# Kernel tuning notes

Measured on AMD Instinct MI355X. Metric: run time of the kernel, lower is better.

The kernel has to match this reference:

```python
import jax, jax.numpy as jnp
import numpy as np

INPUT_DIM = 2048
N_TREES = 15
TREE_DEPTH = 3
N_LEAVES = 2 ** TREE_DEPTH          # 8
N_INTERNAL = 2 ** TREE_DEPTH - 1    # 7
PARAM_PER_TREE = N_INTERNAL * (INPUT_DIM + 1) + N_LEAVES * 2  # 14375
BATCH = 32768


def setup_inputs() -> dict:
    key = jax.random.key(0)
    k1, k2, k3 = jax.random.split(key, 3)
    x = jax.random.normal(k1, (BATCH, INPUT_DIM), dtype=jnp.float32)
    tree_params = jax.random.normal(k2, (1, N_TREES * PARAM_PER_TREE), dtype=jnp.float32)
    tree_weights = jax.random.uniform(k3, (1, N_TREES), dtype=jnp.float32)
    return {"x": x, "tree_params": tree_params, "tree_weights": tree_weights}


def reference(x, tree_params, tree_weights):
    D, T, I, L = INPUT_DIM, N_TREES, N_INTERNAL, N_LEAVES
    B = x.shape[0]
    p = tree_params[0].reshape(T, PARAM_PER_TREE)
    split_w = p[:, : I * D].reshape(T, I, D)                       # [T, I, D]
    split_b = p[:, I * D : I * (D + 1)]                            # [T, I]
    leaf_logits = p[:, I * (D + 1) :].reshape(T, L, 2)             # [T, L, 2]

    # One fused GEMM over all trees/nodes: [B, T, I]
    decisions = jax.nn.sigmoid(jnp.einsum('bd,tid->bti', x, split_w) + split_b)

    # Faithful replication of the original gating loop (leaf 0 ungated,
    # internal nodes with child index >= L are no-ops).
    leaf_probs = jnp.ones((B, T, L), dtype=x.dtype)
    for i in range(I):
        left, right = 2 * i + 1, 2 * i + 2
        d = decisions[:, :, i]
        if left < L:
            leaf_probs = leaf_probs.at[:, :, left].multiply(d)
        if right < L:
            leaf_probs = leaf_probs.at[:, :, right].multiply(1.0 - d)

    leaf_probs = leaf_probs / (leaf_probs.sum(axis=-1, keepdims=True) + 1e-8)
    leaf_dist = jax.nn.softmax(leaf_logits, axis=-1)               # [T, L, 2]
    tree_out = jnp.einsum('btl,tlc->btc', leaf_probs, leaf_dist)   # [B, T, 2]
    final_probs = jnp.einsum('btc,t->bc', tree_out, tree_weights[0])
    return final_probs
```

## Files before the change

### kernel.cpp

```cpp
#include <hip/hip_runtime.h>
#include <stdint.h>

#define D_IN    2048
#define NT      15
#define PPT     14359
#define NVALID  60

typedef __bf16   bf16x8 __attribute__((ext_vector_type(8)));
typedef float    f32x4  __attribute__((ext_vector_type(4)));
typedef uint32_t u32x4  __attribute__((ext_vector_type(4)));

#define WAITV(n) asm volatile("s_waitcnt vmcnt(" #n ")" ::: "memory")
#define WAITL0   asm volatile("s_waitcnt lgkmcnt(0)" ::: "memory")
#define SCHEDB   __builtin_amdgcn_sched_barrier(0)

#define CVT_PAIR(P, Q, HW, LW) do {                                   \
    uint32_t _up = __float_as_uint(P), _uq = __float_as_uint(Q);      \
    uint32_t _mp = _up & 0xFFFF0000u, _mq = _uq & 0xFFFF0000u;        \
    (HW) = (_up >> 16) | _mq;                                         \
    float _lp = (P) - __uint_as_float(_mp);                           \
    float _lq = (Q) - __uint_as_float(_mq);                           \
    (LW) = (__float_as_uint(_lp) >> 16) |                             \
           (__float_as_uint(_lq) & 0xFFFF0000u);                      \
  } while (0)

__device__ __forceinline__ void cvt8(const f32x4 A, const f32x4 B,
                                     u32x4& hi, u32x4& lo) {
  CVT_PAIR(A[0], A[1], hi[0], lo[0]);
  CVT_PAIR(A[2], A[3], hi[1], lo[1]);
  CVT_PAIR(B[0], B[1], hi[2], lo[2]);
  CVT_PAIR(B[2], B[3], hi[3], lo[3]);
}

__global__ __launch_bounds__(256) void prep_split(const float* __restrict__ tp,
                                                  const float* __restrict__ tw,
                                                  unsigned short* __restrict__ bsp,
                                                  float* __restrict__ bias,
                                                  float* __restrict__ coef) {
  const int n  = blockIdx.x;
  const int j  = threadIdx.x;
  const int k0 = j * 8;
  f32x4 v0 = {0,0,0,0}, v1 = {0,0,0,0};
  if (n < NVALID) {
    const float* src = tp + (size_t)(n >> 2) * PPT + (n & 3) * D_IN + k0;
#pragma unroll
    for (int q = 0; q < 4; ++q) v0[q] = src[q];
#pragma unroll
    for (int q = 0; q < 4; ++q) v1[q] = src[4 + q];
  }
  u32x4 hi, lo;
  cvt8(v0, v1, hi, lo);
  const int ks = k0 >> 5, f = n >> 4;
  const int lane = (n & 15) | (((k0 >> 3) & 3) << 4);
  char* bb = (char*)bsp + ((size_t)(ks * 4 + f) * 2) * 1024 + (size_t)lane * 16;
  *(u32x4*)(bb)        = hi;
  *(u32x4*)(bb + 1024) = lo;

  if (blockIdx.x == 0) {
    int tid = threadIdx.x;
    if (tid < 64) {
      float b = 0.0f;
      if (tid < NVALID) { int t = tid >> 2, i = tid & 3; b = tp[t * PPT + 14336 + i]; }
      bias[tid] = b;
    } else if (tid < 64 + NT) {
      int t = tid - 64;
      const float* ll = tp + t * PPT + 14343;
      float d0[8], d1[8];
#pragma unroll
      for (int le = 0; le < 8; ++le) {
        float aa = ll[2 * le], bb2 = ll[2 * le + 1];
        float m = fmaxf(aa, bb2);
        float e0 = __expf(aa - m), e1 = __expf(bb2 - m);
        float inv = 1.0f / (e0 + e1);
        d0[le] = e0 * inv; d1[le] = e1 * inv;
      }
      float ww = tw[t];
      float* c = coef + t * 10;
      c[0] = ww * (d0[0] + d0[2] + d0[4] + d0[6]);
      c[1] = ww * (d1[0] + d1[2] + d1[4] + d1[6]);
      c[2] = ww * (d0[1] - d0[2]);
      c[3] = ww * (d1[1] - d1[2]);
      c[4] = ww * (d0[3] - d0[4]);
      c[5] = ww * (d1[3] - d1[4]);
      c[6] = ww * (d0[5] - d0[6]);
      c[7] = ww * (d1[5] - d1[6]);
      c[8] = ww * d0[7];
      c[9] = ww * d1[7];
    }
  }
}

__device__ __forceinline__ f32x4 gload4(const float* p) {
  f32x4 r;
  asm volatile("global_load_dwordx4 %0, %1, off" : "=v"(r) : "v"(p) : "memory");
  return r;
}
__device__ __forceinline__ u32x4 dsread16(uint32_t addr) {
  u32x4 r;
  asm volatile("ds_read_b128 %0, %1" : "=v"(r) : "v"(addr) : "memory");
  return r;
}
__device__ __forceinline__ void stage16(const void* g, void* l) {
  __builtin_amdgcn_global_load_lds(
      (const __attribute__((address_space(1))) void*)g,
      (__attribute__((address_space(3))) void*)l, 16, 0, 0);
}

#define ITERATION(tt, BUF, RC, WN, ISSUE)                                      \
  {                                                                            \
    WAITV(WN); SCHEDB;                                                         \
    __builtin_amdgcn_s_barrier();                                              \
    const uint32_t bb = sbase + (BUF) * 16384 + l16;                           \
    u32x4 bfr[16];                                                             \
    _Pragma("unroll")                                                          \
    for (int q = 0; q < 16; ++q) bfr[q] = dsread16(bb + q * 1024);             \
    u32x4 ah0, al0, ah1, al1;                                                  \
    cvt8(RC[0], RC[1], ah0, al0);                                              \
    cvt8(RC[2], RC[3], ah1, al1);                                              \
    WAITL0; SCHEDB;                                                            \
    if (ISSUE) {                                                               \
      const int t3 = (tt) + 3;                                                 \
      const char* gsrc = bspb + (size_t)t3 * 16384 + w4096l16;                 \
      char* ldst = sBgen + (((BUF) + 3) & 3) * 16384 + w4096;                  \
      _Pragma("unroll")                                                        \
      for (int q = 0; q < 4; ++q) stage16(gsrc + q * 1024, ldst + q * 1024);   \
      const float* ap = xbase + t3 * 64;                                       \
      RC[0] = gload4(ap);      RC[1] = gload4(ap + 4);                         \
      RC[2] = gload4(ap + 32); RC[3] = gload4(ap + 36);                        \
    }                                                                          \
    _Pragma("unroll")                                                          \
    for (int f = 0; f < 4; ++f) {                                              \
      bf16x8 bh = __builtin_bit_cast(bf16x8, bfr[f * 2]);                      \
      bf16x8 bl = __builtin_bit_cast(bf16x8, bfr[f * 2 + 1]);                  \
      bf16x8 Ah = __builtin_bit_cast(bf16x8, ah0);                             \
      bf16x8 Al = __builtin_bit_cast(bf16x8, al0);                             \
      acc[f] = __builtin_amdgcn_mfma_f32_16x16x32_bf16(Ah, bh, acc[f], 0,0,0); \
      acc[f] = __builtin_amdgcn_mfma_f32_16x16x32_bf16(Al, bh, acc[f], 0,0,0); \
      acc[f] = __builtin_amdgcn_mfma_f32_16x16x32_bf16(Ah, bl, acc[f], 0,0,0); \
    }                                                                          \
    _Pragma("unroll")                                                          \
    for (int f = 0; f < 4; ++f) {                                              \
      bf16x8 bh = __builtin_bit_cast(bf16x8, bfr[8 + f * 2]);                  \
      bf16x8 bl = __builtin_bit_cast(bf16x8, bfr[8 + f * 2 + 1]);              \
      bf16x8 Ah = __builtin_bit_cast(bf16x8, ah1);                             \
      bf16x8 Al = __builtin_bit_cast(bf16x8, al1);                             \
      acc[f] = __builtin_amdgcn_mfma_f32_16x16x32_bf16(Ah, bh, acc[f], 0,0,0); \
      acc[f] = __builtin_amdgcn_mfma_f32_16x16x32_bf16(Al, bh, acc[f], 0,0,0); \
      acc[f] = __builtin_amdgcn_mfma_f32_16x16x32_bf16(Ah, bl, acc[f], 0,0,0); \
    }                                                                          \
  }

__global__ __launch_bounds__(256) void tree_fused(
    const float* __restrict__ x,
    const unsigned short* __restrict__ bsp,
    const float* __restrict__ bias,
    const float* __restrict__ coef,
    float* __restrict__ out)
{
  __shared__ __align__(1024) unsigned char sB[4 * 16384];

  const int tid = threadIdx.x;
  const int w   = tid >> 6;
  const int l   = tid & 63;
  const int rl  = l & 15;
  const int g   = l >> 4;
  const int l16 = l * 16;
  const int w4096 = w * 4096;
  const int w4096l16 = w4096 + l16;

  const int rowTile = blockIdx.x * 64 + w * 16;
  const float* xbase = x + (size_t)(rowTile + rl) * D_IN + g * 8;
  const char* bspb = (const char*)bsp;
  char* sBgen = (char*)&sB[0];
  const uint32_t sbase = (uint32_t)(uintptr_t)sBgen;

  f32x4 acc[4] = {};
  f32x4 r0[4], r1[4], r2[4];

  {
#pragma unroll
    for (int s = 0; s < 3; ++s) {
      const char* gs = bspb + (size_t)s * 16384 + w4096l16;
      char* ld = sBgen + s * 16384 + w4096;
#pragma unroll
      for (int q = 0; q < 4; ++q) stage16(gs + q * 1024, ld + q * 1024);
      const float* ap = xbase + s * 64;
      f32x4* rr = (s == 0) ? r0 : (s == 1) ? r1 : r2;
      rr[0] = gload4(ap);      rr[1] = gload4(ap + 4);
      rr[2] = gload4(ap + 32); rr[3] = gload4(ap + 36);
    }
  }

  for (int tb = 0; tb < 24; tb += 12) {
    ITERATION(tb + 0,  0, r0, 16, 1);
    ITERATION(tb + 1,  1, r1, 16, 1);
    ITERATION(tb + 2,  2, r2, 16, 1);
    ITERATION(tb + 3,  3, r0, 16, 1);
    ITERATION(tb + 4,  0, r1, 16, 1);
    ITERATION(tb + 5,  1, r2, 16, 1);
    ITERATION(tb + 6,  2, r0, 16, 1);
    ITERATION(tb + 7,  3, r1, 16, 1);
    ITERATION(tb + 8,  0, r2, 16, 1);
    ITERATION(tb + 9,  1, r0, 16, 1);
    ITERATION(tb + 10, 2, r1, 16, 1);
    ITERATION(tb + 11, 3, r2, 16, 1);
  }
  ITERATION(24, 0, r0, 16, 1);
  ITERATION(25, 1, r1, 16, 1);
  ITERATION(26, 2, r2, 16, 1);
  ITERATION(27, 3, r0, 16, 1);
  ITERATION(28, 0, r1, 16, 1);
  ITERATION(29, 1, r2, 16, 0);
  ITERATION(30, 2, r0,  8, 0);
  ITERATION(31, 3, r1,  0, 0);

  float (*strips)[16][65] = (float (*)[16][65])sBgen;
#pragma unroll
  for (int f = 0; f < 4; ++f)
#pragma unroll
    for (int r = 0; r < 4; ++r)
      strips[w][4 * g + r][16 * f + rl] = acc[f][r];
  WAITL0;

  float o0 = 0.0f, o1 = 0.0f;
#pragma unroll
  for (int jt = 0; jt < 4; ++jt) {
    int t = g + 4 * jt;
    if (t < NT) {
      const float* cf = coef + t * 10;
      float dd[4];
#pragma unroll
      for (int i = 0; i < 4; ++i) {
        float z = strips[w][rl][4 * t + i] + bias[4 * t + i];
        dd[i] = 1.0f / (1.0f + __expf(-z));
      }
      float s = 1.0f / (4.0f + dd[3] + 1e-8f);
      o0 += s * (cf[0] + dd[0] * cf[2] + dd[1] * cf[4] + dd[2] * cf[6] + dd[3] * cf[8]);
      o1 += s * (cf[1] + dd[0] * cf[3] + dd[1] * cf[5] + dd[2] * cf[7] + dd[3] * cf[9]);
    }
  }
  o0 += __shfl_xor(o0, 16); o0 += __shfl_xor(o0, 32);
  o1 += __shfl_xor(o1, 16); o1 += __shfl_xor(o1, 32);
  if (l < 16) {
    ((float2*)out)[rowTile + rl] = make_float2(o0, o1);
  }
}

extern "C" void kernel_launch(void* const* d_in, const int* in_sizes, int n_in,
                              void* d_out, int out_size, void* d_ws, size_t ws_size,
                              hipStream_t stream) {
  (void)in_sizes; (void)n_in; (void)out_size; (void)ws_size;
  const float* x  = (const float*)d_in[0];
  const float* tp = (const float*)d_in[1];
  const float* tw = (const float*)d_in[2];
  float* out = (float*)d_out;

  unsigned short* bsp = (unsigned short*)d_ws;
  float* bias = (float*)((char*)d_ws + 524288);
  float* coef = (float*)((char*)d_ws + 524288 + 256);

  prep_split<<<64, 256, 0, stream>>>(tp, tw, bsp, bias, coef);
  tree_fused<<<512, 256, 0, stream>>>(x, bsp, bias, coef, out);
}
```

Before: 57.33 us.

## Split N dimension across two wave groups with 512-thread blocks and 3-stage buffer

Doubles the block to 8 waves. Each 16-row M tile is now shared by two waves, and each of those waves computes half of the 64 output columns, so accumulators and B-fragment registers per wave are halved. The LDS pipeline drops from 4 stages to 3 (prefetch distance 2 instead of 3), which frees shared memory and registers so more waves can be resident. In exchange, every x row is loaded and converted twice (once per N-half), a full __syncthreads is needed before the epilogue, and per-half partial outputs are reduced through LDS.

```diff
diff --git a/kernel.cpp b/kernel.cpp
--- a/kernel.cpp
+++ b/kernel.cpp
@@ -110,128 +110,120 @@
   {                                                                            \
     WAITV(WN); SCHEDB;                                                         \
     __builtin_amdgcn_s_barrier();                                              \
-    const uint32_t bb = sbase + (BUF) * 16384 + l16;                           \
-    u32x4 bfr[16];                                                             \
-    _Pragma("unroll")                                                          \
-    for (int q = 0; q < 16; ++q) bfr[q] = dsread16(bb + q * 1024);             \
+    const uint32_t bb = sbase + (BUF) * 16384 + n4096 + l16;                   \
+    u32x4 bfr[8];                                                              \
+    _Pragma("unroll")                                                          \
+    for (int q = 0; q < 4; ++q) bfr[q]     = dsread16(bb + q * 1024);          \
+    _Pragma("unroll")                                                          \
+    for (int q = 0; q < 4; ++q) bfr[4 + q] = dsread16(bb + 8192 + q * 1024);   \
     u32x4 ah0, al0, ah1, al1;                                                  \
     cvt8(RC[0], RC[1], ah0, al0);                                              \
     cvt8(RC[2], RC[3], ah1, al1);                                              \
     WAITL0; SCHEDB;                                                            \
     if (ISSUE) {                                                               \
-      const int t3 = (tt) + 3;                                                 \
-      const char* gsrc = bspb + (size_t)t3 * 16384 + w4096l16;                 \
-      char* ldst = sBgen + (((BUF) + 3) & 3) * 16384 + w4096;                  \
-      _Pragma("unroll")                                                        \
-      for (int q = 0; q < 4; ++q) stage16(gsrc + q * 1024, ldst + q * 1024);   \
-      const float* ap = xbase + t3 * 64;                                       \
+      const int t2 = (tt) + 2;                                                 \
+      const char* gsrc = bspb + (size_t)t2 * 16384 + w2048l16;                 \
+      char* ldst = sBgen + (((BUF) + 2) % 3) * 16384 + w2048;                  \
+      stage16(gsrc,        ldst);                                              \
+      stage16(gsrc + 1024, ldst + 1024);                                       \
+      const float* ap = xbase + t2 * 64;                                       \
       RC[0] = gload4(ap);      RC[1] = gload4(ap + 4);                         \
       RC[2] = gload4(ap + 32); RC[3] = gload4(ap + 36);                        \
     }                                                                          \
     _Pragma("unroll")                                                          \
-    for (int f = 0; f < 4; ++f) {                                              \
-      bf16x8 bh = __builtin_bit_cast(bf16x8, bfr[f * 2]);                      \
-      bf16x8 bl = __builtin_bit_cast(bf16x8, bfr[f * 2 + 1]);                  \
+    for (int ff = 0; ff < 2; ++ff) {                                           \
+      bf16x8 bh = __builtin_bit_cast(bf16x8, bfr[2 * ff]);                     \
+      bf16x8 bl = __builtin_bit_cast(bf16x8, bfr[2 * ff + 1]);                 \
       bf16x8 Ah = __builtin_bit_cast(bf16x8, ah0);                             \
       bf16x8 Al = __builtin_bit_cast(bf16x8, al0);                             \
-      acc[f] = __builtin_amdgcn_mfma_f32_16x16x32_bf16(Ah, bh, acc[f], 0,0,0); \
-      acc[f] = __builtin_amdgcn_mfma_f32_16x16x32_bf16(Al, bh, acc[f], 0,0,0); \
-      acc[f] = __builtin_amdgcn_mfma_f32_16x16x32_bf16(Ah, bl, acc[f], 0,0,0); \
+      acc[ff] = __builtin_amdgcn_mfma_f32_16x16x32_bf16(Ah, bh, acc[ff],0,0,0);\
+      acc[ff] = __builtin_amdgcn_mfma_f32_16x16x32_bf16(Al, bh, acc[ff],0,0,0);\
+      acc[ff] = __builtin_amdgcn_mfma_f32_16x16x32_bf16(Ah, bl, acc[ff],0,0,0);\
     }                                                                          \
     _Pragma("unroll")                                                          \
-    for (int f = 0; f < 4; ++f) {                                              \
-      bf16x8 bh = __builtin_bit_cast(bf16x8, bfr[8 + f * 2]);                  \
-      bf16x8 bl = __builtin_bit_cast(bf16x8, bfr[8 + f * 2 + 1]);              \
+    for (int ff = 0; ff < 2; ++ff) {                                           \
+      bf16x8 bh = __builtin_bit_cast(bf16x8, bfr[4 + 2 * ff]);                 \
+      bf16x8 bl = __builtin_bit_cast(bf16x8, bfr[4 + 2 * ff + 1]);             \
       bf16x8 Ah = __builtin_bit_cast(bf16x8, ah1);                             \
       bf16x8 Al = __builtin_bit_cast(bf16x8, al1);                             \
-      acc[f] = __builtin_amdgcn_mfma_f32_16x16x32_bf16(Ah, bh, acc[f], 0,0,0); \
-      acc[f] = __builtin_amdgcn_mfma_f32_16x16x32_bf16(Al, bh, acc[f], 0,0,0); \
-      acc[f] = __builtin_amdgcn_mfma_f32_16x16x32_bf16(Ah, bl, acc[f], 0,0,0); \
+      acc[ff] = __builtin_amdgcn_mfma_f32_16x16x32_bf16(Ah, bh, acc[ff],0,0,0);\
+      acc[ff] = __builtin_amdgcn_mfma_f32_16x16x32_bf16(Al, bh, acc[ff],0,0,0);\
+      acc[ff] = __builtin_amdgcn_mfma_f32_16x16x32_bf16(Ah, bl, acc[ff],0,0,0);\
     }                                                                          \
   }
 
-__global__ __launch_bounds__(256) void tree_fused(
+__global__ __launch_bounds__(512, 4) void tree_fused(
     const float* __restrict__ x,
     const unsigned short* __restrict__ bsp,
     const float* __restrict__ bias,
     const float* __restrict__ coef,
     float* __restrict__ out)
 {
-  __shared__ __align__(1024) unsigned char sB[4 * 16384];
+  __shared__ __align__(1024) unsigned char sB[3 * 16384];
 
   const int tid = threadIdx.x;
   const int w   = tid >> 6;
   const int l   = tid & 63;
   const int rl  = l & 15;
   const int g   = l >> 4;
+  const int m   = w & 3;
+  const int n   = w >> 2;
   const int l16 = l * 16;
-  const int w4096 = w * 4096;
-  const int w4096l16 = w4096 + l16;
-
-  const int rowTile = blockIdx.x * 64 + w * 16;
+  const int n4096 = n * 4096;
+  const int w2048 = w * 2048;
+  const int w2048l16 = w2048 + l16;
+
+  const int rowTile = blockIdx.x * 64 + m * 16;
   const float* xbase = x + (size_t)(rowTile + rl) * D_IN + g * 8;
   const char* bspb = (const char*)bsp;
   char* sBgen = (char*)&sB[0];
   const uint32_t sbase = (uint32_t)(uintptr_t)sBgen;
 
-  f32x4 acc[4] = {};
-  f32x4 r0[4], r1[4], r2[4];
+  f32x4 acc[2] = {};
+  f32x4 rA[4], rB[4];
 
   {
-#pragma unroll
-    for (int s = 0; s < 3; ++s) {
-      const char* gs = bspb + (size_t)s * 16384 + w4096l16;
-      char* ld = sBgen + s * 16384 + w4096;
-#pragma unroll
-      for (int q = 0; q < 4; ++q) stage16(gs + q * 1024, ld + q * 1024);
-      const float* ap = xbase + s * 64;
-      f32x4* rr = (s == 0) ? r0 : (s == 1) ? r1 : r2;
-      rr[0] = gload4(ap);      rr[1] = gload4(ap + 4);
-      rr[2] = gload4(ap + 32); rr[3] = gload4(ap + 36);
-    }
-  }
-
-  for (int tb = 0; tb < 24; tb += 12) {
-    ITERATION(tb + 0,  0, r0, 16, 1);
-    ITERATION(tb + 1,  1, r1, 16, 1);
-    ITERATION(tb + 2,  2, r2, 16, 1);
-    ITERATION(tb + 3,  3, r0, 16, 1);
-    ITERATION(tb + 4,  0, r1, 16, 1);
-    ITERATION(tb + 5,  1, r2, 16, 1);
-    ITERATION(tb + 6,  2, r0, 16, 1);
-    ITERATION(tb + 7,  3, r1, 16, 1);
-    ITERATION(tb + 8,  0, r2, 16, 1);
-    ITERATION(tb + 9,  1, r0, 16, 1);
-    ITERATION(tb + 10, 2, r1, 16, 1);
-    ITERATION(tb + 11, 3, r2, 16, 1);
-  }
-  ITERATION(24, 0, r0, 16, 1);
-  ITERATION(25, 1, r1, 16, 1);
-  ITERATION(26, 2, r2, 16, 1);
-  ITERATION(27, 3, r0, 16, 1);
-  ITERATION(28, 0, r1, 16, 1);
-  ITERATION(29, 1, r2, 16, 0);
-  ITERATION(30, 2, r0,  8, 0);
-  ITERATION(31, 3, r1,  0, 0);
-
-  float (*strips)[16][65] = (float (*)[16][65])sBgen;
-#pragma unroll
-  for (int f = 0; f < 4; ++f)
+    stage16(bspb + w2048l16,        sBgen + w2048);
+    stage16(bspb + w2048l16 + 1024, sBgen + w2048 + 1024);
+    rA[0] = gload4(xbase);      rA[1] = gload4(xbase + 4);
+    rA[2] = gload4(xbase + 32); rA[3] = gload4(xbase + 36);
+    stage16(bspb + 16384 + w2048l16,        sBgen + 16384 + w2048);
+    stage16(bspb + 16384 + w2048l16 + 1024, sBgen + 16384 + w2048 + 1024);
+    rB[0] = gload4(xbase + 64); rB[1] = gload4(xbase + 68);
+    rB[2] = gload4(xbase + 96); rB[3] = gload4(xbase + 100);
+  }
+
+  for (int tb = 0; tb < 30; tb += 6) {
+    ITERATION(tb + 0, 0, rA, 6, 1);
+    ITERATION(tb + 1, 1, rB, 6, 1);
+    ITERATION(tb + 2, 2, rA, 6, 1);
+    ITERATION(tb + 3, 0, rB, 6, 1);
+    ITERATION(tb + 4, 1, rA, 6, 1);
+    ITERATION(tb + 5, 2, rB, 6, 1);
+  }
+  ITERATION(30, 0, rA, 6, 0);
+  ITERATION(31, 1, rB, 0, 0);
+
+  float* sfl = (float*)sBgen;
+  float* pp  = (float*)(sBgen + 2 * 16384);
+
+#pragma unroll
+  for (int ff = 0; ff < 2; ++ff)
 #pragma unroll
     for (int r = 0; r < 4; ++r)
-      strips[w][4 * g + r][16 * f + rl] = acc[f][r];
-  WAITL0;
+      sfl[(m * 16 + 4 * g + r) * 64 + 32 * n + 16 * ff + rl] = acc[ff][r];
+  __syncthreads();
 
   float o0 = 0.0f, o1 = 0.0f;
 #pragma unroll
-  for (int jt = 0; jt < 4; ++jt) {
-    int t = g + 4 * jt;
+  for (int jt2 = 0; jt2 < 2; ++jt2) {
+    int t = g + 4 * (2 * n + jt2);
     if (t < NT) {
       const float* cf = coef + t * 10;
       float dd[4];
 #pragma unroll
       for (int i = 0; i < 4; ++i) {
-        float z = strips[w][rl][4 * t + i] + bias[4 * t + i];
+        float z = sfl[(m * 16 + rl) * 64 + 4 * t + i] + bias[4 * t + i];
         dd[i] = 1.0f / (1.0f + __expf(-z));
       }
       float s = 1.0f / (4.0f + dd[3] + 1e-8f);
@@ -242,7 +234,14 @@
   o0 += __shfl_xor(o0, 16); o0 += __shfl_xor(o0, 32);
   o1 += __shfl_xor(o1, 16); o1 += __shfl_xor(o1, 32);
   if (l < 16) {
-    ((float2*)out)[rowTile + rl] = make_float2(o0, o1);
+    pp[((m * 2 + n) * 16 + rl) * 2 + 0] = o0;
+    pp[((m * 2 + n) * 16 + rl) * 2 + 1] = o1;
+  }
+  __syncthreads();
+  if (n == 0 && l < 16) {
+    float a0 = pp[((m * 2) * 16 + rl) * 2 + 0] + pp[((m * 2 + 1) * 16 + rl) * 2 + 0];
+    float a1 = pp[((m * 2) * 16 + rl) * 2 + 1] + pp[((m * 2 + 1) * 16 + rl) * 2 + 1];
+    ((float2*)out)[rowTile + rl] = make_float2(a0, a1);
   }
 }
 
@@ -260,5 +259,5 @@
   float* coef = (float*)((char*)d_ws + 524288 + 256);
 
   prep_split<<<64, 256, 0, stream>>>(tp, tw, bsp, bias, coef);
-  tree_fused<<<512, 256, 0, stream>>>(x, bsp, bias, coef, out);
-}
+  tree_fused<<<512, 512, 0, stream>>>(x, bsp, bias, coef, out);
+}
```

After: 81.23 us. 41.7% more time.

## Swap operand staging: stream B into registers, stage x through swizzled LDS

Applied to the files above, without the earlier changes.

The weight tile (B) is now double-buffered directly in registers via global loads that every wave issues (each wave reads the full 16 KB per k-step), instead of being shared through LDS with block barriers. The x rows are staged per-wave into a 3-deep swizzled LDS ring via global_load_lds and read back with ds_read_b128. This removes the per-iteration s_barrier and the 16 LDS reads of B per step. In exchange it raises VGPR pressure (64 u32x4 registers for B buffers) and multiplies global and L2 traffic for B by four, which may hurt occupancy.

```diff
diff --git a/kernel.cpp b/kernel.cpp
--- a/kernel.cpp
+++ b/kernel.cpp
@@ -90,8 +90,13 @@
   }
 }
 
-__device__ __forceinline__ f32x4 gload4(const float* p) {
+__device__ __forceinline__ f32x4 gload4f(const float* p) {
   f32x4 r;
+  asm volatile("global_load_dwordx4 %0, %1, off" : "=v"(r) : "v"(p) : "memory");
+  return r;
+}
+__device__ __forceinline__ u32x4 gload4u(const char* p) {
+  u32x4 r;
   asm volatile("global_load_dwordx4 %0, %1, off" : "=v"(r) : "v"(p) : "memory");
   return r;
 }
@@ -106,47 +111,59 @@
       (__attribute__((address_space(3))) void*)l, 16, 0, 0);
 }
 
-#define ITERATION(tt, BUF, RC, WN, ISSUE)                                      \
+#define ITERATION(tt, AB, BC0, BC1, BN0, BN1, W3, W6, ISSA, ISSB)              \
   {                                                                            \
-    WAITV(WN); SCHEDB;                                                         \
-    __builtin_amdgcn_s_barrier();                                              \
-    const uint32_t bb = sbase + (BUF) * 16384 + l16;                           \
-    u32x4 bfr[16];                                                             \
-    _Pragma("unroll")                                                          \
-    for (int q = 0; q < 16; ++q) bfr[q] = dsread16(bb + q * 1024);             \
-    u32x4 ah0, al0, ah1, al1;                                                  \
-    cvt8(RC[0], RC[1], ah0, al0);                                              \
-    cvt8(RC[2], RC[3], ah1, al1);                                              \
+    if (ISSA) {                                                                \
+      const int t2 = (tt) + 2;                                                 \
+      char* ldst = sAw + (((AB) + 2) % 3) * 4096;                              \
+      stage16(xsb0 + t2 * 64, ldst);                                           \
+      stage16(xsb1 + t2 * 64, ldst + 1024);                                    \
+      stage16(xsb2 + t2 * 64, ldst + 2048);                                    \
+      stage16(xsb3 + t2 * 64, ldst + 3072);                                    \
+    }                                                                          \
+    WAITV(W3); SCHEDB;                                                         \
+    const uint32_t ab_ = sabase + (AB) * 4096;                                 \
+    u32x4 ar0 = dsread16(ab_ + sw0a);                                          \
+    u32x4 ar1 = dsread16(ab_ + sw0b);                                          \
+    u32x4 ar2 = dsread16(ab_ + sw1a);                                          \
+    u32x4 ar3 = dsread16(ab_ + sw1b);                                          \
     WAITL0; SCHEDB;                                                            \
-    if (ISSUE) {                                                               \
-      const int t3 = (tt) + 3;                                                 \
-      const char* gsrc = bspb + (size_t)t3 * 16384 + w4096l16;                 \
-      char* ldst = sBgen + (((BUF) + 3) & 3) * 16384 + w4096;                  \
-      _Pragma("unroll")                                                        \
-      for (int q = 0; q < 4; ++q) stage16(gsrc + q * 1024, ldst + q * 1024);   \
-      const float* ap = xbase + t3 * 64;                                       \
-      RC[0] = gload4(ap);      RC[1] = gload4(ap + 4);                         \
-      RC[2] = gload4(ap + 32); RC[3] = gload4(ap + 36);                        \
-    }                                                                          \
+    u32x4 ah0, al0;                                                            \
+    cvt8(__builtin_bit_cast(f32x4, ar0), __builtin_bit_cast(f32x4, ar1),       \
+         ah0, al0);                                                            \
     _Pragma("unroll")                                                          \
     for (int f = 0; f < 4; ++f) {                                              \
-      bf16x8 bh = __builtin_bit_cast(bf16x8, bfr[f * 2]);                      \
-      bf16x8 bl = __builtin_bit_cast(bf16x8, bfr[f * 2 + 1]);                  \
+      bf16x8 bh = __builtin_bit_cast(bf16x8, BC0[2 * f]);                      \
+      bf16x8 bl = __builtin_bit_cast(bf16x8, BC0[2 * f + 1]);                  \
       bf16x8 Ah = __builtin_bit_cast(bf16x8, ah0);                             \
       bf16x8 Al = __builtin_bit_cast(bf16x8, al0);                             \
       acc[f] = __builtin_amdgcn_mfma_f32_16x16x32_bf16(Ah, bh, acc[f], 0,0,0); \
       acc[f] = __builtin_amdgcn_mfma_f32_16x16x32_bf16(Al, bh, acc[f], 0,0,0); \
       acc[f] = __builtin_amdgcn_mfma_f32_16x16x32_bf16(Ah, bl, acc[f], 0,0,0); \
     }                                                                          \
+    if (ISSB) {                                                                \
+      const char* bsrc = bspb + (size_t)((tt) + 1) * 16384 + l16;              \
+      _Pragma("unroll")                                                        \
+      for (int q = 0; q < 8; ++q) BN0[q] = gload4u(bsrc + q * 1024);           \
+    }                                                                          \
+    WAITV(W6); SCHEDB;                                                         \
+    u32x4 ah1, al1;                                                            \
+    cvt8(__builtin_bit_cast(f32x4, ar2), __builtin_bit_cast(f32x4, ar3),       \
+         ah1, al1);                                                            \
     _Pragma("unroll")                                                          \
     for (int f = 0; f < 4; ++f) {                                              \
-      bf16x8 bh = __builtin_bit_cast(bf16x8, bfr[8 + f * 2]);                  \
-      bf16x8 bl = __builtin_bit_cast(bf16x8, bfr[8 + f * 2 + 1]);              \
+      bf16x8 bh = __builtin_bit_cast(bf16x8, BC1[2 * f]);                      \
+      bf16x8 bl = __builtin_bit_cast(bf16x8, BC1[2 * f + 1]);                  \
       bf16x8 Ah = __builtin_bit_cast(bf16x8, ah1);                             \
       bf16x8 Al = __builtin_bit_cast(bf16x8, al1);                             \
       acc[f] = __builtin_amdgcn_mfma_f32_16x16x32_bf16(Ah, bh, acc[f], 0,0,0); \
       acc[f] = __builtin_amdgcn_mfma_f32_16x16x32_bf16(Al, bh, acc[f], 0,0,0); \
       acc[f] = __builtin_amdgcn_mfma_f32_16x16x32_bf16(Ah, bl, acc[f], 0,0,0); \
+    }                                                                          \
+    if (ISSB) {                                                                \
+      const char* bsrc = bspb + (size_t)((tt) + 1) * 16384 + l16;              \
+      _Pragma("unroll")                                                        \
+      for (int q = 0; q < 8; ++q) BN1[q] = gload4u(bsrc + (8 + q) * 1024);     \
     }                                                                          \
   }
 
@@ -157,7 +174,8 @@
     const float* __restrict__ coef,
     float* __restrict__ out)
 {
-  __shared__ __align__(1024) unsigned char sB[4 * 16384];
+  __shared__ __align__(1024) unsigned char sA[4 * 3 * 4096];
+  __shared__ float strips[4][16][65];
 
   const int tid = threadIdx.x;
   const int w   = tid >> 6;
@@ -165,56 +183,52 @@
   const int rl  = l & 15;
   const int g   = l >> 4;
   const int l16 = l * 16;
-  const int w4096 = w * 4096;
-  const int w4096l16 = w4096 + l16;
+  const int r7  = rl & 7;
 
   const int rowTile = blockIdx.x * 64 + w * 16;
-  const float* xbase = x + (size_t)(rowTile + rl) * D_IN + g * 8;
   const char* bspb = (const char*)bsp;
-  char* sBgen = (char*)&sB[0];
-  const uint32_t sbase = (uint32_t)(uintptr_t)sBgen;
+  char* sAw = (char*)&sA[0] + w * 12288;
+  const uint32_t sabase = (uint32_t)(uintptr_t)sAw;
+
+  const uint32_t sw0a = (uint32_t)rl * 256 + (uint32_t)(((2 * g + 0) ^ r7) << 4);
+  const uint32_t sw0b = (uint32_t)rl * 256 + (uint32_t)(((2 * g + 1) ^ r7) << 4);
+  const uint32_t sw1a = (uint32_t)rl * 256 + (uint32_t)(((8 + 2 * g + 0) ^ r7) << 4);
+  const uint32_t sw1b = (uint32_t)rl * 256 + (uint32_t)(((8 + 2 * g + 1) ^ r7) << 4);
+
+  const int sr0 = 0 * 4 + (l >> 4), sr1 = 1 * 4 + (l >> 4);
+  const int sr2 = 2 * 4 + (l >> 4), sr3 = 3 * 4 + (l >> 4);
+  const float* xsb0 = x + (size_t)(rowTile + sr0) * D_IN + (((l & 15) ^ (sr0 & 7)) << 2);
+  const float* xsb1 = x + (size_t)(rowTile + sr1) * D_IN + (((l & 15) ^ (sr1 & 7)) << 2);
+  const float* xsb2 = x + (size_t)(rowTile + sr2) * D_IN + (((l & 15) ^ (sr2 & 7)) << 2);
+  const float* xsb3 = x + (size_t)(rowTile + sr3) * D_IN + (((l & 15) ^ (sr3 & 7)) << 2);
 
   f32x4 acc[4] = {};
-  f32x4 r0[4], r1[4], r2[4];
+  u32x4 be0[8], be1[8], bo0[8], bo1[8];
 
   {
-#pragma unroll
-    for (int s = 0; s < 3; ++s) {
-      const char* gs = bspb + (size_t)s * 16384 + w4096l16;
-      char* ld = sBgen + s * 16384 + w4096;
-#pragma unroll
-      for (int q = 0; q < 4; ++q) stage16(gs + q * 1024, ld + q * 1024);
-      const float* ap = xbase + s * 64;
-      f32x4* rr = (s == 0) ? r0 : (s == 1) ? r1 : r2;
-      rr[0] = gload4(ap);      rr[1] = gload4(ap + 4);
-      rr[2] = gload4(ap + 32); rr[3] = gload4(ap + 36);
-    }
-  }
-
-  for (int tb = 0; tb < 24; tb += 12) {
-    ITERATION(tb + 0,  0, r0, 16, 1);
-    ITERATION(tb + 1,  1, r1, 16, 1);
-    ITERATION(tb + 2,  2, r2, 16, 1);
-    ITERATION(tb + 3,  3, r0, 16, 1);
-    ITERATION(tb + 4,  0, r1, 16, 1);
-    ITERATION(tb + 5,  1, r2, 16, 1);
-    ITERATION(tb + 6,  2, r0, 16, 1);
-    ITERATION(tb + 7,  3, r1, 16, 1);
-    ITERATION(tb + 8,  0, r2, 16, 1);
-    ITERATION(tb + 9,  1, r0, 16, 1);
-    ITERATION(tb + 10, 2, r1, 16, 1);
-    ITERATION(tb + 11, 3, r2, 16, 1);
-  }
-  ITERATION(24, 0, r0, 16, 1);
-  ITERATION(25, 1, r1, 16, 1);
-  ITERATION(26, 2, r2, 16, 1);
-  ITERATION(27, 3, r0, 16, 1);
-  ITERATION(28, 0, r1, 16, 1);
-  ITERATION(29, 1, r2, 16, 0);
-  ITERATION(30, 2, r0,  8, 0);
-  ITERATION(31, 3, r1,  0, 0);
-
-  float (*strips)[16][65] = (float (*)[16][65])sBgen;
+    stage16(xsb0, sAw);            stage16(xsb1, sAw + 1024);
+    stage16(xsb2, sAw + 2048);     stage16(xsb3, sAw + 3072);
+    stage16(xsb0 + 64, sAw + 4096);        stage16(xsb1 + 64, sAw + 4096 + 1024);
+    stage16(xsb2 + 64, sAw + 4096 + 2048); stage16(xsb3 + 64, sAw + 4096 + 3072);
+    const char* bsrc = bspb + l16;
+#pragma unroll
+    for (int q = 0; q < 8; ++q) be0[q] = gload4u(bsrc + q * 1024);
+#pragma unroll
+    for (int q = 0; q < 8; ++q) be1[q] = gload4u(bsrc + (8 + q) * 1024);
+  }
+  __syncthreads();
+
+  for (int tb = 0; tb < 30; tb += 6) {
+    ITERATION(tb + 0, 0, be0, be1, bo0, bo1, 12, 12, 1, 1);
+    ITERATION(tb + 1, 1, bo0, bo1, be0, be1, 12, 12, 1, 1);
+    ITERATION(tb + 2, 2, be0, be1, bo0, bo1, 12, 12, 1, 1);
+    ITERATION(tb + 3, 0, bo0, bo1, be0, be1, 12, 12, 1, 1);
+    ITERATION(tb + 4, 1, be0, be1, bo0, bo1, 12, 12, 1, 1);
+    ITERATION(tb + 5, 2, bo0, bo1, be0, be1, 12, 12, 1, 1);
+  }
+  ITERATION(30, 0, be0, be1, bo0, bo1, 8, 8, 0, 1);
+  ITERATION(31, 1, bo0, bo1, be0, be1, 8, 0, 0, 0);
+
 #pragma unroll
   for (int f = 0; f < 4; ++f)
 #pragma unroll
```

After: 67.75 us. 1.18x slower.

## Split K across two blocks with partial-sum workspace and separate finish kernel

Applied to the files above, without the earlier changes.

Each row tile is now processed by two blocks, each covering half of the 2048-wide reduction with half-size LDS stages and x loads per iteration. Partial GEMM results go to a global workspace, and a new finish kernel sums the two halves and applies the sigmoid/leaf epilogue. The goal is twice as many blocks with smaller LDS footprint for more occupancy and latency hiding on the memory-bound x stream. The cost is extra global traffic for partials and an additional kernel launch.

```diff
diff --git a/kernel.cpp b/kernel.cpp
--- a/kernel.cpp
+++ b/kernel.cpp
@@ -50,9 +50,9 @@
   }
   u32x4 hi, lo;
   cvt8(v0, v1, hi, lo);
-  const int ks = k0 >> 5, f = n >> 4;
+  const int s = k0 >> 5, f = n >> 4;
   const int lane = (n & 15) | (((k0 >> 3) & 3) << 4);
-  char* bb = (char*)bsp + ((size_t)(ks * 4 + f) * 2) * 1024 + (size_t)lane * 16;
+  char* bb = (char*)bsp + (size_t)s * 8192 + (size_t)f * 2048 + (size_t)lane * 16;
   *(u32x4*)(bb)        = hi;
   *(u32x4*)(bb + 1024) = lo;
 
@@ -110,54 +110,40 @@
   {                                                                            \
     WAITV(WN); SCHEDB;                                                         \
     __builtin_amdgcn_s_barrier();                                              \
-    const uint32_t bb = sbase + (BUF) * 16384 + l16;                           \
-    u32x4 bfr[16];                                                             \
+    const uint32_t bb = sbase + (BUF) * 8192 + l16;                            \
+    u32x4 bfr[8];                                                              \
     _Pragma("unroll")                                                          \
-    for (int q = 0; q < 16; ++q) bfr[q] = dsread16(bb + q * 1024);             \
-    u32x4 ah0, al0, ah1, al1;                                                  \
-    cvt8(RC[0], RC[1], ah0, al0);                                              \
-    cvt8(RC[2], RC[3], ah1, al1);                                              \
+    for (int q = 0; q < 8; ++q) bfr[q] = dsread16(bb + q * 1024);              \
+    u32x4 ah, al;                                                              \
+    cvt8(RC[0], RC[1], ah, al);                                                \
     WAITL0; SCHEDB;                                                            \
     if (ISSUE) {                                                               \
       const int t3 = (tt) + 3;                                                 \
-      const char* gsrc = bspb + (size_t)t3 * 16384 + w4096l16;                 \
-      char* ldst = sBgen + (((BUF) + 3) & 3) * 16384 + w4096;                  \
-      _Pragma("unroll")                                                        \
-      for (int q = 0; q < 4; ++q) stage16(gsrc + q * 1024, ldst + q * 1024);   \
-      const float* ap = xbase + t3 * 64;                                       \
-      RC[0] = gload4(ap);      RC[1] = gload4(ap + 4);                         \
-      RC[2] = gload4(ap + 32); RC[3] = gload4(ap + 36);                        \
+      const char* gsrc = bspb + (size_t)t3 * 8192 + w2048l16;                  \
+      char* ldst = sBgen + (((BUF) + 3) & 3) * 8192 + w2048;                   \
+      stage16(gsrc,        ldst);                                              \
+      stage16(gsrc + 1024, ldst + 1024);                                       \
+      const float* ap = xbase + t3 * 32;                                       \
+      RC[0] = gload4(ap);  RC[1] = gload4(ap + 4);                             \
     }                                                                          \
     _Pragma("unroll")                                                          \
     for (int f = 0; f < 4; ++f) {                                              \
       bf16x8 bh = __builtin_bit_cast(bf16x8, bfr[f * 2]);                      \
       bf16x8 bl = __builtin_bit_cast(bf16x8, bfr[f * 2 + 1]);                  \
-      bf16x8 Ah = __builtin_bit_cast(bf16x8, ah0);                             \
-      bf16x8 Al = __builtin_bit_cast(bf16x8, al0);                             \
+      bf16x8 Ah = __builtin_bit_cast(bf16x8, ah);                              \
+      bf16x8 Al = __builtin_bit_cast(bf16x8, al);                              \
       acc[f] = __builtin_amdgcn_mfma_f32_16x16x32_bf16(Ah, bh, acc[f], 0,0,0); \
       acc[f] = __builtin_amdgcn_mfma_f32_16x16x32_bf16(Al, bh, acc[f], 0,0,0); \
       acc[f] = __builtin_amdgcn_mfma_f32_16x16x32_bf16(Ah, bl, acc[f], 0,0,0); \
     }                                                                          \
-    _Pragma("unroll")                                                          \
-    for (int f = 0; f < 4; ++f) {                                              \
-      bf16x8 bh = __builtin_bit_cast(bf16x8, bfr[8 + f * 2]);                  \
-      bf16x8 bl = __builtin_bit_cast(bf16x8, bfr[8 + f * 2 + 1]);              \
-      bf16x8 Ah = __builtin_bit_cast(bf16x8, ah1);                             \
-      bf16x8 Al = __builtin_bit_cast(bf16x8, al1);                             \
-      acc[f] = __builtin_amdgcn_mfma_f32_16x16x32_bf16(Ah, bh, acc[f], 0,0,0); \
-      acc[f] = __builtin_amdgcn_mfma_f32_16x16x32_bf16(Al, bh, acc[f], 0,0,0); \
-      acc[f] = __builtin_amdgcn_mfma_f32_16x16x32_bf16(Ah, bl, acc[f], 0,0,0); \
-    }                                                                          \
-  }
-
-__global__ __launch_bounds__(256) void tree_fused(
+  }
+
+__global__ __launch_bounds__(256, 4) void tree_gemm(
     const float* __restrict__ x,
     const unsigned short* __restrict__ bsp,
-    const float* __restrict__ bias,
-    const float* __restrict__ coef,
-    float* __restrict__ out)
+    float* __restrict__ pws)
 {
-  __shared__ __align__(1024) unsigned char sB[4 * 16384];
+  __shared__ __align__(1024) unsigned char sB[4 * 8192];
 
   const int tid = threadIdx.x;
   const int w   = tid >> 6;
@@ -165,62 +151,87 @@
   const int rl  = l & 15;
   const int g   = l >> 4;
   const int l16 = l * 16;
-  const int w4096 = w * 4096;
-  const int w4096l16 = w4096 + l16;
-
-  const int rowTile = blockIdx.x * 64 + w * 16;
-  const float* xbase = x + (size_t)(rowTile + rl) * D_IN + g * 8;
-  const char* bspb = (const char*)bsp;
+  const int w2048 = w * 2048;
+  const int w2048l16 = w2048 + l16;
+
+  const int tile = blockIdx.x >> 1;
+  const int kh   = blockIdx.x & 1;
+  const int rowTile = tile * 64 + w * 16;
+  const float* xbase = x + (size_t)(rowTile + rl) * D_IN + kh * 1024 + g * 8;
+  const char* bspb = (const char*)bsp + (size_t)kh * 32 * 8192;
   char* sBgen = (char*)&sB[0];
   const uint32_t sbase = (uint32_t)(uintptr_t)sBgen;
 
   f32x4 acc[4] = {};
-  f32x4 r0[4], r1[4], r2[4];
+  f32x4 r0[2], r1[2], r2[2];
 
   {
 #pragma unroll
     for (int s = 0; s < 3; ++s) {
-      const char* gs = bspb + (size_t)s * 16384 + w4096l16;
-      char* ld = sBgen + s * 16384 + w4096;
-#pragma unroll
-      for (int q = 0; q < 4; ++q) stage16(gs + q * 1024, ld + q * 1024);
-      const float* ap = xbase + s * 64;
+      const char* gs = bspb + (size_t)s * 8192 + w2048l16;
+      char* ld = sBgen + s * 8192 + w2048;
+      stage16(gs, ld);
+      stage16(gs + 1024, ld + 1024);
+      const float* ap = xbase + s * 32;
       f32x4* rr = (s == 0) ? r0 : (s == 1) ? r1 : r2;
-      rr[0] = gload4(ap);      rr[1] = gload4(ap + 4);
-      rr[2] = gload4(ap + 32); rr[3] = gload4(ap + 36);
+      rr[0] = gload4(ap);  rr[1] = gload4(ap + 4);
     }
   }
 
   for (int tb = 0; tb < 24; tb += 12) {
-    ITERATION(tb + 0,  0, r0, 16, 1);
-    ITERATION(tb + 1,  1, r1, 16, 1);
-    ITERATION(tb + 2,  2, r2, 16, 1);
-    ITERATION(tb + 3,  3, r0, 16, 1);
-    ITERATION(tb + 4,  0, r1, 16, 1);
-    ITERATION(tb + 5,  1, r2, 16, 1);
-    ITERATION(tb + 6,  2, r0, 16, 1);
-    ITERATION(tb + 7,  3, r1, 16, 1);
-    ITERATION(tb + 8,  0, r2, 16, 1);
-    ITERATION(tb + 9,  1, r0, 16, 1);
-    ITERATION(tb + 10, 2, r1, 16, 1);
-    ITERATION(tb + 11, 3, r2, 16, 1);
-  }
-  ITERATION(24, 0, r0, 16, 1);
-  ITERATION(25, 1, r1, 16, 1);
-  ITERATION(26, 2, r2, 16, 1);
-  ITERATION(27, 3, r0, 16, 1);
-  ITERATION(28, 0, r1, 16, 1);
-  ITERATION(29, 1, r2, 16, 0);
-  ITERATION(30, 2, r0,  8, 0);
-  ITERATION(31, 3, r1,  0, 0);
-
-  float (*strips)[16][65] = (float (*)[16][65])sBgen;
+    ITERATION(tb + 0,  0, r0, 8, 1);
+    ITERATION(tb + 1,  1, r1, 8, 1);
+    ITERATION(tb + 2,  2, r2, 8, 1);
+    ITERATION(tb + 3,  3, r0, 8, 1);
+    ITERATION(tb + 4,  0, r1, 8, 1);
+    ITERATION(tb + 5,  1, r2, 8, 1);
+    ITERATION(tb + 6,  2, r0, 8, 1);
+    ITERATION(tb + 7,  3, r1, 8, 1);
+    ITERATION(tb + 8,  0, r2, 8, 1);
+    ITERATION(tb + 9,  1, r0, 8, 1);
+    ITERATION(tb + 10, 2, r1, 8, 1);
+    ITERATION(tb + 11, 3, r2, 8, 1);
+  }
+  ITERATION(24, 0, r0, 8, 1);
+  ITERATION(25, 1, r1, 8, 1);
+  ITERATION(26, 2, r2, 8, 1);
+  ITERATION(27, 3, r0, 8, 1);
+  ITERATION(28, 0, r1, 8, 1);
+  ITERATION(29, 1, r2, 8, 0);
+  ITERATION(30, 2, r0, 4, 0);
+  ITERATION(31, 3, r1, 0, 0);
+
+  float* pb = pws + (size_t)blockIdx.x * 4096;
 #pragma unroll
   for (int f = 0; f < 4; ++f)
 #pragma unroll
     for (int r = 0; r < 4; ++r)
-      strips[w][4 * g + r][16 * f + rl] = acc[f][r];
-  WAITL0;
+      pb[(w * 16 + 4 * g + r) * 64 + 16 * f + rl] = acc[f][r];
+}
+
+__global__ __launch_bounds__(256) void tree_finish(
+    const float* __restrict__ pws,
+    const float* __restrict__ bias,
+    const float* __restrict__ coef,
+    float* __restrict__ out)
+{
+  __shared__ float strip[64][65];
+
+  const int tid = threadIdx.x;
+  const int w   = tid >> 6;
+  const int l   = tid & 63;
+  const int rl  = l & 15;
+  const int g   = l >> 4;
+  const int tile = blockIdx.x;
+
+  const float* p0 = pws + (size_t)tile * 8192;
+  const float* p1 = p0 + 4096;
+#pragma unroll
+  for (int i = 0; i < 16; ++i) {
+    int idx = i * 256 + tid;
+    strip[idx >> 6][idx & 63] = p0[idx] + p1[idx];
+  }
+  __syncthreads();
 
   float o0 = 0.0f, o1 = 0.0f;
 #pragma unroll
@@ -231,7 +242,7 @@
       float dd[4];
 #pragma unroll
       for (int i = 0; i < 4; ++i) {
-        float z = strips[w][rl][4 * t + i] + bias[4 * t + i];
+        float z = strip[w * 16 + rl][4 * t + i] + bias[4 * t + i];
         dd[i] = 1.0f / (1.0f + __expf(-z));
       }
       float s = 1.0f / (4.0f + dd[3] + 1e-8f);
@@ -242,7 +253,7 @@
   o0 += __shfl_xor(o0, 16); o0 += __shfl_xor(o0, 32);
   o1 += __shfl_xor(o1, 16); o1 += __shfl_xor(o1, 32);
   if (l < 16) {
-    ((float2*)out)[rowTile + rl] = make_float2(o0, o1);
+    ((float2*)out)[tile * 64 + w * 16 + rl] = make_float2(o0, o1);
   }
 }
 
@@ -256,9 +267,11 @@
   float* out = (float*)d_out;
 
   unsigned short* bsp = (unsigned short*)d_ws;
-  float* bias = (float*)((char*)d_ws + 524288);
-  float* coef = (float*)((char*)d_ws + 524288 + 256);
+  float* pws  = (float*)((char*)d_ws + 524288);
+  float* bias = (float*)((char*)d_ws + 524288 + 16777216);
+  float* coef = (float*)((char*)d_ws + 524288 + 16777216 + 256);
 
   prep_split<<<64, 256, 0, stream>>>(tp, tw, bsp, bias, coef);
-  tree_fused<<<512, 256, 0, stream>>>(x, bsp, bias, coef, out);
-}
+  tree_gemm<<<1024, 256, 0, stream>>>(x, bsp, pws);
+  tree_finish<<<512, 256, 0, stream>>>(pws, bias, coef, out);
+}
```

After: 78.77 us. +37.4%, slower.
